# Kernel optimization log

Hardware: AMD Instinct MI355X
Metric: run time of the kernel (lower is better)

The kernel has to match this reference:

```python
import jax, jax.numpy as jnp
import numpy as np

MAX_TOTAL = 20        # max_total_size
MAX_PER_CLASS = 20    # max_output_size_per_class
SCORE_TH = 0.5        # score_threshold
IOU_TH = 0.5          # tf combined NMS default iou_threshold
K_CAND = 200          # top candidates per class considered for NMS
VARIANCES = jnp.array([0.1, 0.1, 0.2, 0.2], jnp.float32)


def setup_inputs() -> dict:
    key = jax.random.key(0)
    k1, k2, k3, k4, k5, k6 = jax.random.split(key, 6)
    B, N, C = 64, 8732, 21
    pred_deltas = jax.random.normal(k1, (B, N, 4), jnp.float32)
    pred_labels = jax.random.uniform(k2, (B, N, C), dtype=jnp.float32)
    # synthetic normalized anchors (y1,x1,y2,x2) with valid extents
    cy = jax.random.uniform(k3, (N,), dtype=jnp.float32)
    cx = jax.random.uniform(k4, (N,), dtype=jnp.float32)
    h = jax.random.uniform(k5, (N,), dtype=jnp.float32, minval=0.05, maxval=0.3)
    w = jax.random.uniform(k6, (N,), dtype=jnp.float32, minval=0.05, maxval=0.3)
    anchors = jnp.stack([cy - h / 2, cx - w / 2, cy + h / 2, cx + w / 2], axis=-1)
    return {"pred_deltas": pred_deltas, "pred_labels": pred_labels, "anchors": anchors}


def _decode(anchors, deltas):
    # anchors [N,4] (y1,x1,y2,x2); deltas [B,N,4] (dy,dx,dh,dw) -> boxes [B,N,4]
    ah = anchors[:, 2] - anchors[:, 0]
    aw = anchors[:, 3] - anchors[:, 1]
    acy = anchors[:, 0] + 0.5 * ah
    acx = anchors[:, 1] + 0.5 * aw
    cy = deltas[..., 0] * ah + acy
    cx = deltas[..., 1] * aw + acx
    h = jnp.exp(deltas[..., 2]) * ah
    w = jnp.exp(deltas[..., 3]) * aw
    return jnp.stack([cy - 0.5 * h, cx - 0.5 * w, cy + 0.5 * h, cx + 0.5 * w], axis=-1)


def _pairwise_iou(boxes):
    # boxes [K,4] -> iou [K,K]
    y1, x1, y2, x2 = boxes[:, 0], boxes[:, 1], boxes[:, 2], boxes[:, 3]
    area = (y2 - y1) * (x2 - x1)
    ih = jnp.clip(jnp.minimum(y2[:, None], y2[None, :]) - jnp.maximum(y1[:, None], y1[None, :]), 0.0)
    iw = jnp.clip(jnp.minimum(x2[:, None], x2[None, :]) - jnp.maximum(x1[:, None], x1[None, :]), 0.0)
    inter = ih * iw
    return inter / (area[:, None] + area[None, :] - inter + 1e-8)


def _nms_one_class(scores, boxes):
    # scores [N], boxes [N,4] -> (top scores [MAX_PER_CLASS], boxes [MAX_PER_CLASS,4])
    vals, idx = jax.lax.top_k(scores, K_CAND)          # sorted desc
    cboxes = boxes[idx]                                # [K,4]
    iou = _pairwise_iou(cboxes)                        # [K,K]
    valid = vals > SCORE_TH
    ar = jnp.arange(K_CAND)

    def body(i, keep):
        suppressed = jnp.any(keep & (iou[i] > IOU_TH) & (ar < i))
        return keep.at[i].set(valid[i] & ~suppressed)

    keep = jax.lax.fori_loop(0, K_CAND, body, jnp.zeros(K_CAND, dtype=bool))
    kept_scores = jnp.where(keep, vals, 0.0)
    top_vals, top_i = jax.lax.top_k(kept_scores, MAX_PER_CLASS)
    return top_vals, cboxes[top_i]


def reference(pred_deltas, pred_labels, anchors):
    deltas = pred_deltas * VARIANCES                       # variance scaling
    boxes = _decode(anchors, deltas)                       # [B,N,4]
    # zero out all class scores where argmax class == 0 (background)
    lab_map = jnp.argmax(pred_labels, axis=-1, keepdims=True)
    scores = jnp.where(lab_map != 0, pred_labels, 0.0)     # [B,N,C]

    per_class = jax.vmap(_nms_one_class, in_axes=(1, None))   # over classes
    per_batch = jax.vmap(per_class, in_axes=(0, 0))           # over batch
    cls_scores, cls_boxes = per_batch(scores, boxes)          # [B,C,P], [B,C,P,4]

    B, C, P = cls_scores.shape
    flat_scores = cls_scores.reshape(B, C * P)
    flat_boxes = cls_boxes.reshape(B, C * P, 4)
    class_ids = jnp.broadcast_to(jnp.arange(C, dtype=jnp.float32)[:, None], (C, P)).reshape(-1)

    top_vals, top_i = jax.lax.top_k(flat_scores, MAX_TOTAL)   # [B,MAX_TOTAL]
    final_boxes = jnp.take_along_axis(flat_boxes, top_i[..., None], axis=1)
    final_boxes = jnp.clip(final_boxes, 0.0, 1.0)             # combined NMS clip_boxes=True
    valid = top_vals > 0.0
    final_boxes = jnp.where(valid[..., None], final_boxes, 0.0)
    final_labels = jnp.where(valid, class_ids[top_i], 0.0)
    return final_boxes, top_vals, final_labels
```

## Files before the change

### kernel.cpp

```cpp
#include <hip/hip_runtime.h>
#include <stdint.h>

typedef unsigned long long u64;
typedef unsigned int u32;
typedef unsigned short u16;

#define BATCH 64
#define NANCH 8732
#define NCHUNK 1092
#define NCLS 21
#define KCAND 200
#define CAP 2048
#define PPC 20
#define PTOT 20
#define PRETHR 0.9f

__global__ __launch_bounds__(256) void kzero(u32* __restrict__ cnt)
{
    int i = blockIdx.x * 256 + threadIdx.x;
    if (i < BATCH * NCLS) cnt[i] = 0;
}

__global__ __launch_bounds__(256) void kdecode(
    const float* __restrict__ labels,
    unsigned char* __restrict__ msk, u64* __restrict__ lists,
    u32* __restrict__ cnt, int useT)
{
#pragma clang fp contract(off)
    const int n = blockIdx.x * 256 + threadIdx.x;
    const int b = blockIdx.y;
    const int lane = threadIdx.x & 63;
    const bool active = (n < NANCH);

    float v[NCLS];
#pragma unroll
    for (int c = 0; c < NCLS; ++c) v[c] = 0.0f;
    bool mk = false;
    if (active) {
        const float* lab = labels + ((size_t)b * NANCH + n) * NCLS;
#pragma unroll
        for (int c = 0; c < NCLS; ++c) v[c] = lab[c];
        float mx = v[0]; int am = 0;
#pragma unroll
        for (int c = 1; c < NCLS; ++c) if (v[c] > mx) { mx = v[c]; am = c; }
        mk = (am != 0);
        msk[(size_t)b * NANCH + n] = mk ? 1 : 0;
    }
    if (!useT) return;

    u32 myHits = 0;
#pragma unroll
    for (int c = 0; c < NCLS; ++c)
        if (active && mk && v[c] >= PRETHR) myHits |= (1u << c);

    u32 myCnt = 0;
#pragma unroll
    for (int c = 0; c < NCLS; ++c) {
        u64 m = __ballot((myHits >> c) & 1u);
        if (lane == c) myCnt = (u32)__popcll(m);
    }
    u32 myBase = 0;
    if (lane < NCLS) myBase = atomicAdd(&cnt[b * NCLS + lane], myCnt);

#pragma unroll
    for (int c = 0; c < NCLS; ++c) {
        u64 m = __ballot((myHits >> c) & 1u);
        u32 base = (u32)__shfl((int)myBase, c, 64);
        if ((m >> lane) & 1ull) {
            u32 rank = (u32)__popcll(m & ((1ull << lane) - 1ull));
            u32 slot = base + rank;
            if (slot < CAP)
                lists[((size_t)b * NCLS + c) * CAP + slot] =
                    ((u64)__float_as_uint(v[c]) << 32) | (u32)(~(u32)n);
        }
    }
}

__device__ __forceinline__ u64 shflxor64(u64 x, int m) {
    return (u64)__shfl_xor((long long)x, m, 64);
}

__device__ __forceinline__ void suffixFind(const u32* hist, u32* waveTot, int nb, int need,
                                           int* sSel, int* sAbove, int* sH, int* sTot,
                                           int tid, int lane, int wv)
{
    int K = (nb + 255) >> 8;
    int base = tid * K;
    u32 own = 0;
    for (int q = 0; q < K; ++q) { int bi = base + q; own += (bi < nb) ? hist[bi] : 0u; }
    u32 s = own;
#pragma unroll
    for (int d = 1; d < 64; d <<= 1) {
        u32 o = __shfl_down(s, d, 64);
        if (lane + d < 64) s += o;
    }
    if (lane == 0) waveTot[wv] = s;
    __syncthreads();
    if (tid == 0 && sTot) *sTot = (int)(waveTot[0] + waveTot[1] + waveTot[2] + waveTot[3]);
    u32 add = 0;
    for (int w = wv + 1; w < 4; ++w) add += waveTot[w];
    u32 cum = (s - own) + add;
    for (int q = K - 1; q >= 0; --q) {
        int bi = base + q;
        u32 hh = (bi < nb) ? hist[bi] : 0u;
        if (cum < (u32)need && cum + hh >= (u32)need) { *sSel = bi; *sAbove = (int)cum; *sH = (int)hh; }
        cum += hh;
    }
    __syncthreads();
}

__global__ __launch_bounds__(256) void knms(
    const float* __restrict__ labels, const unsigned char* __restrict__ msk,
    const u64* __restrict__ lists, const u32* __restrict__ cnt,
    const float* __restrict__ deltas, const float* __restrict__ anchors,
    float* __restrict__ clsScores, float* __restrict__ clsBoxes, int useT)
{
#pragma clang fp contract(off)
    __shared__ __align__(16) char smem[8192];
    u32*   hist = (u32*)smem;
    float* cbY1 = (float*)smem;
    float* cbX1 = (float*)(smem + 1024);
    float* cbY2 = (float*)(smem + 2048);
    float* cbX2 = (float*)(smem + 3072);
    float* cbAr = (float*)(smem + 4096);
    float* cVal = (float*)(smem + 5120);
    u64*   iouT = (u64*)(smem + 6144);
    __shared__ u64 candKey[256];
    __shared__ u32 waveTot[4];
    __shared__ float outS[PPC];
    __shared__ float outB[PPC * 4];
    __shared__ int sSel, sAbove, sH, sTot, sN, sKP;

    const int tid = threadIdx.x;
    const int lane = tid & 63;
    const int wv = tid >> 6;
    const int bc = blockIdx.x;
    const int b = bc / NCLS;
    const int c = bc % NCLS;

    const int nTHR = useT ? (int)cnt[bc] : -1;
    const bool fast = useT && (nTHR >= KCAND) && (nTHR <= CAP);

    if (fast) {
        const u64* lst = lists + (size_t)bc * CAP;
        u64 kr[8];
#pragma unroll
        for (int q = 0; q < 8; ++q) {
            int i = q * 256 + tid;
            kr[q] = (i < nTHR) ? lst[i] : 0ull;
        }
        for (int q = tid; q < 1024; q += 256) hist[1024 + q] = 0;
        if (tid == 0) { sSel = -1; sAbove = 0; sH = 0; sN = 0; sKP = 0; }
        __syncthreads();
#pragma unroll
        for (int q = 0; q < 8; ++q) {
            if (q * 256 + tid < nTHR) {
                float v = __uint_as_float((u32)(kr[q] >> 32));
                u32 t = (u32)(v * 65536.0f);
                atomicAdd(&hist[t >> 5], 1u);
            }
        }
        __syncthreads();
        suffixFind(hist + 1024, waveTot, 1024, KCAND, &sSel, &sAbove, &sH, nullptr, tid, lane, wv);
        int A = sAbove;
        u32 T16 = (u32)(1024 + sSel) << 5;
        int cnt2 = A + sH;

        if (cnt2 > 256) {
            if (tid < 32) hist[tid] = 0;
            if (tid == 0) { sSel = -1; sAbove = 0; sH = 0; }
            __syncthreads();
#pragma unroll
            for (int q = 0; q < 8; ++q) {
                if (q * 256 + tid < nTHR) {
                    float v = __uint_as_float((u32)(kr[q] >> 32));
                    u32 t = (u32)(v * 65536.0f);
                    if (t >= T16 && t < T16 + 32) atomicAdd(&hist[t - T16], 1u);
                }
            }
            __syncthreads();
            suffixFind(hist, waveTot, 32, KCAND - A, &sSel, &sAbove, &sH, nullptr, tid, lane, wv);
            A += sAbove;
            T16 += (u32)sSel;
        }
#pragma unroll
        for (int q = 0; q < 8; ++q) {
            if (q * 256 + tid < nTHR) {
                float v = __uint_as_float((u32)(kr[q] >> 32));
                u32 t = (u32)(v * 65536.0f);
                if (t >= T16) {
                    int slot = atomicAdd(&sN, 1);
                    if (slot < 256) candKey[slot] = kr[q];
                }
            }
        }
    } else {
        uint4 rc[5];
        for (int q = 0; q < 5; ++q) {
            int chunk = q * 256 + tid;
            u32 w4[4] = {0, 0, 0, 0};
            if (chunk < NCHUNK) {
                for (int w = 0; w < 4; ++w)
                    for (int h = 0; h < 2; ++h) {
                        int n = chunk * 8 + w * 2 + h;
                        u32 t = 0;
                        if (n < NANCH && msk[(size_t)b * NANCH + n]) {
                            float v = labels[((size_t)b * NANCH + n) * NCLS + c];
                            t = (u32)(v * 65536.0f);
                        }
                        w4[w] |= t << (16 * h);
                    }
            }
            rc[q] = make_uint4(w4[0], w4[1], w4[2], w4[3]);
        }
        for (int q = tid; q < 1024; q += 256) hist[1024 + q] = 0;
        if (tid == 0) { sSel = -1; sAbove = 0; sH = 0; sTot = 0; sN = 0; sKP = 0; }
        __syncthreads();
#pragma unroll
        for (int q = 0; q < 5; ++q) {
            if (q * 256 + tid < NCHUNK) {
                u32 w4[4] = {rc[q].x, rc[q].y, rc[q].z, rc[q].w};
#pragma unroll
                for (int w = 0; w < 4; ++w) {
                    u32 lo = w4[w] & 0xFFFFu, hi = w4[w] >> 16;
                    if (lo & 0x8000u) atomicAdd(&hist[lo >> 5], 1u);
                    if (hi & 0x8000u) atomicAdd(&hist[hi >> 5], 1u);
                }
            }
        }
        __syncthreads();
        suffixFind(hist + 1024, waveTot, 1024, KCAND, &sSel, &sAbove, &sH, &sTot, tid, lane, wv);
        int A; int cnt2; u32 T16;
        if (sTot < KCAND) { T16 = 32768u; A = 0; cnt2 = sTot; }
        else { A = sAbove; T16 = (u32)(1024 + sSel) << 5; cnt2 = A + sH; }
        if (cnt2 > 256) {
            if (tid < 32) hist[tid] = 0;
            if (tid == 0) { sSel = -1; sAbove = 0; sH = 0; }
            __syncthreads();
#pragma unroll
            for (int q = 0; q < 5; ++q) {
                if (q * 256 + tid < NCHUNK) {
                    u32 w4[4] = {rc[q].x, rc[q].y, rc[q].z, rc[q].w};
#pragma unroll
                    for (int w = 0; w < 4; ++w) {
                        u32 lo = w4[w] & 0xFFFFu, hi = w4[w] >> 16;
                        if (lo >= T16 && lo < T16 + 32) atomicAdd(&hist[lo - T16], 1u);
                        if (hi >= T16 && hi < T16 + 32) atomicAdd(&hist[hi - T16], 1u);
                    }
                }
            }
            __syncthreads();
            suffixFind(hist, waveTot, 32, KCAND - A, &sSel, &sAbove, &sH, nullptr, tid, lane, wv);
            A += sAbove;
            T16 += (u32)sSel;
        }
#pragma unroll
        for (int q = 0; q < 5; ++q) {
            int chunk = q * 256 + tid;
            if (chunk < NCHUNK) {
                u32 w4[4] = {rc[q].x, rc[q].y, rc[q].z, rc[q].w};
#pragma unroll
                for (int w = 0; w < 4; ++w) {
#pragma unroll
                    for (int h = 0; h < 2; ++h) {
                        u32 t = (h == 0) ? (w4[w] & 0xFFFFu) : (w4[w] >> 16);
                        if (t >= T16) {
                            int n = chunk * 8 + w * 2 + h;
                            float v = labels[((size_t)b * NANCH + n) * NCLS + c];
                            int slot = atomicAdd(&sN, 1);
                            if (slot < 256)
                                candKey[slot] = ((u64)__float_as_uint(v) << 32) | (u32)(~(u32)n);
                        }
                    }
                }
            }
        }
    }
    __syncthreads();
    int nc = sN; if (nc > 256) nc = 256;

    u64 x = (tid < nc) ? candKey[tid] : 0ull;
    for (int k = 2; k <= 256; k <<= 1) {
        for (int j = k >> 1; j > 0; j >>= 1) {
            u64 y;
            if (j < 64) {
                y = shflxor64(x, j);
            } else {
                __syncthreads();
                candKey[tid] = x;
                __syncthreads();
                y = candKey[tid ^ j];
            }
            bool keepMax = ((tid & k) == 0) == ((tid & j) == 0);
            u64 mx = (x > y) ? x : y;
            u64 mn = (x > y) ? y : x;
            x = keepMax ? mx : mn;
        }
    }

    float myV = __uint_as_float((u32)(x >> 32));
    float myY1 = 0.f, myX1 = 0.f, myY2 = 0.f, myX2 = 0.f, myAr = 0.f;
    u32 idx = ~(u32)x;
    if (tid < KCAND && idx < (u32)NANCH) {
        float4 d = ((const float4*)deltas)[(size_t)b * NANCH + idx];
        float4 a = ((const float4*)anchors)[idx];
        float ah = a.z - a.x, aw = a.w - a.y;
        float acy = a.x + 0.5f * ah, acx = a.y + 0.5f * aw;
        float cy = (d.x * 0.1f) * ah + acy;
        float cx = (d.y * 0.1f) * aw + acx;
        float hh2 = expf(d.z * 0.2f) * ah;
        float ww2 = expf(d.w * 0.2f) * aw;
        myY1 = cy - 0.5f * hh2; myX1 = cx - 0.5f * ww2;
        myY2 = cy + 0.5f * hh2; myX2 = cx + 0.5f * ww2;
        myAr = (myY2 - myY1) * (myX2 - myX1);
    } else {
        myV = 0.f;
    }
    __syncthreads();
    cbY1[tid] = myY1; cbX1[tid] = myX1; cbY2[tid] = myY2; cbX2[tid] = myX2;
    cbAr[tid] = myAr; cVal[tid] = myV;

    u64 k0 = 0, k1 = 0, k2 = 0, k3 = 0;
    int KPw = 0;
    for (int t0 = 0; t0 < 4; ++t0) {
        __syncthreads();
        if (sKP >= PPC) break;
        int rowBase = t0 * 64;
        int rows = KCAND - rowBase; if (rows > 64) rows = 64;
        for (int r = wv; r < rows; r += 4) {
            int i = rowBase + r;
            float y1i = cbY1[i], x1i = cbX1[i], y2i = cbY2[i], x2i = cbX2[i], ari = cbAr[i];
            for (int cg = 0; cg <= t0; ++cg) {
                int j = cg * 64 + lane;
                float ih = fminf(y2i, cbY2[j]) - fmaxf(y1i, cbY1[j]);
                ih = fmaxf(ih, 0.0f);
                float iw = fminf(x2i, cbX2[j]) - fmaxf(x1i, cbX1[j]);
                iw = fmaxf(iw, 0.0f);
                float inter = ih * iw;
                float iou = inter / (ari + cbAr[j] - inter + 1e-8f);
                u64 bal = __ballot(iou > 0.5f);
                if (lane == 0) iouT[r * 4 + cg] = bal;
            }
        }
        __syncthreads();
        if (tid < 64) {
            int i = rowBase + lane;
            u64 r0 = 0, r1 = 0, r2 = 0, r3 = 0;
            bool vld = false;
            if (lane < rows) {
                r0 = iouT[lane * 4 + 0]; r1 = iouT[lane * 4 + 1];
                r2 = iouT[lane * 4 + 2]; r3 = iouT[lane * 4 + 3];
                vld = cVal[i] > 0.5f;
            }
            for (int l = 0; l < rows; ++l) {
                int mydec = (vld && !((k0 & r0) | (k1 & r1) | (k2 & r2) | (k3 & r3))) ? 1 : 0;
                int d = __shfl(mydec, l, 64);
                if (d) {
                    u64 bit = 1ull << l;
                    if (t0 == 0) k0 |= bit; else if (t0 == 1) k1 |= bit;
                    else if (t0 == 2) k2 |= bit; else k3 |= bit;
                    ++KPw;
                    if (KPw >= PPC) break;
                }
            }
            if (tid == 0) sKP = KPw;
        }
    }
    __syncthreads();

    if (tid < PPC) outS[tid] = 0.0f;
    if (tid < PPC * 4) outB[tid] = 0.0f;
    __syncthreads();

    if (tid < 64) {
        int base = 0;
#pragma unroll
        for (int chunk = 0; chunk < 4; ++chunk) {
            u64 kw = (chunk == 0) ? k0 : (chunk == 1) ? k1 : (chunk == 2) ? k2 : k3;
            int i = chunk * 64 + tid;
            bool kept = ((kw >> tid) & 1ull) != 0;
            int rank = base + (int)__popcll(kw & ((1ull << tid) - 1ull));
            if (kept && rank < PPC && i < KCAND) {
                outS[rank] = cVal[i];
                outB[rank * 4 + 0] = cbY1[i];
                outB[rank * 4 + 1] = cbX1[i];
                outB[rank * 4 + 2] = cbY2[i];
                outB[rank * 4 + 3] = cbX2[i];
            }
            base += (int)__popcll(kw);
        }
    }
    __syncthreads();
    if (tid < PPC) clsScores[(size_t)bc * PPC + tid] = outS[tid];
    if (tid < PPC * 4) clsBoxes[(size_t)bc * PPC * 4 + tid] = outB[tid];
}

__global__ __launch_bounds__(512) void kmerge(
    const float* __restrict__ clsScores, const float* __restrict__ clsBoxes,
    float* __restrict__ out)
{
#pragma clang fp contract(off)
    __shared__ u64 key[512];
    const int tid = threadIdx.x;
    const int b = blockIdx.x;
    const int F = NCLS * PPC;
    u64 kk = 0;
    if (tid < F) {
        float v = clsScores[(size_t)b * F + tid];
        kk = ((u64)__float_as_uint(v) << 32) | (u32)(~(u32)tid);
    }
    key[tid] = kk;
    for (int k = 2; k <= 512; k <<= 1)
        for (int j = k >> 1; j > 0; j >>= 1) {
            __syncthreads();
            int ixj = tid ^ j;
            if (ixj > tid) {
                u64 a = key[tid], bb = key[ixj];
                if (((tid & k) == 0) ? (a < bb) : (a > bb)) { key[tid] = bb; key[ixj] = a; }
            }
        }
    __syncthreads();
    if (tid < PTOT) {
        u64 kx = key[tid];
        float v = __uint_as_float((u32)(kx >> 32));
        u32 f = ~((u32)kx);
        bool valid = (v > 0.0f) && (f < (u32)F);
        float cls = valid ? (float)(f / PPC) : 0.0f;
        float* oB = out;
        float* oV = out + (size_t)BATCH * PTOT * 4;
        float* oL = oV + (size_t)BATCH * PTOT;
#pragma unroll
        for (int q = 0; q < 4; ++q) {
            float xq = 0.0f;
            if (valid) {
                xq = clsBoxes[((size_t)b * F + f) * 4 + q];
                xq = fminf(fmaxf(xq, 0.0f), 1.0f);
            }
            oB[((size_t)b * PTOT + tid) * 4 + q] = xq;
        }
        oV[(size_t)b * PTOT + tid] = v;
        oL[(size_t)b * PTOT + tid] = cls;
    }
}

extern "C" void kernel_launch(void* const* d_in, const int* in_sizes, int n_in,
                              void* d_out, int out_size, void* d_ws, size_t ws_size,
                              hipStream_t stream)
{
    const float* deltas  = (const float*)d_in[0];
    const float* labels  = (const float*)d_in[1];
    const float* anchors = (const float*)d_in[2];
    float* out = (float*)d_out;
    char* ws = (char*)d_ws;

    const size_t mskOff  = 0;
    const size_t cntOff  = 558848;
    const size_t csOff   = 564480;
    const size_t cbOff   = 672000;
    const size_t listOff = 1102336;
    const size_t needT   = 23122432;

    unsigned char* msk = (unsigned char*)(ws + mskOff);
    u32* cnt         = (u32*)(ws + cntOff);
    float* clsScores = (float*)(ws + csOff);
    float* clsBoxes  = (float*)(ws + cbOff);
    u64* lists       = (u64*)(ws + listOff);
    int useT = (ws_size >= needT) ? 1 : 0;

    if (useT) kzero<<<(BATCH * NCLS + 255) / 256, 256, 0, stream>>>(cnt);
    dim3 gA((NANCH + 255) / 256, BATCH);
    kdecode<<<gA, 256, 0, stream>>>(labels, msk, lists, cnt, useT);
    knms<<<BATCH * NCLS, 256, 0, stream>>>(labels, msk, lists, cnt, deltas, anchors,
                                           clsScores, clsBoxes, useT);
    kmerge<<<BATCH, 512, 0, stream>>>(clsScores, clsBoxes, out);
}
```

Measured before the change: 58.55 us.

## Run per-class NMS on a single wavefront to drop block barriers

Each (batch, class) NMS problem now runs on one 64-lane wavefront, with two problems packed per block, so every block-wide barrier becomes a wave-local LDS wait. The histogram suffix search, the candidate bitonic sort (four keys per lane via shuffles) and the greedy suppression loop (broadcasting each kept box by shuffle and testing IoU against register-held boxes) are all rewritten for this layout. The merge kernel's bitonic sort also switches to shuffles for strides below 64. The goal is to cut sync and LDS traffic, at the cost of fewer threads per problem and longer serial loops within each wave.

```diff
diff --git a/kernel.cpp b/kernel.cpp
--- a/kernel.cpp
+++ b/kernel.cpp
@@ -7,13 +7,17 @@
 
 #define BATCH 64
 #define NANCH 8732
-#define NCHUNK 1092
+#define NPAD16 8736
 #define NCLS 21
 #define KCAND 200
 #define CAP 2048
 #define PPC 20
 #define PTOT 20
 #define PRETHR 0.9f
+#define WPB 2
+
+#define WFENCE() do { asm volatile("s_waitcnt lgkmcnt(0)" ::: "memory"); \
+                      __builtin_amdgcn_sched_barrier(0); } while (0)
 
 __global__ __launch_bounds__(256) void kzero(u32* __restrict__ cnt)
 {
@@ -80,350 +84,280 @@
     return (u64)__shfl_xor((long long)x, m, 64);
 }
 
-__device__ __forceinline__ void suffixFind(const u32* hist, u32* waveTot, int nb, int need,
-                                           int* sSel, int* sAbove, int* sH, int* sTot,
-                                           int tid, int lane, int wv)
-{
-    int K = (nb + 255) >> 8;
-    int base = tid * K;
-    u32 own = 0;
-    for (int q = 0; q < K; ++q) { int bi = base + q; own += (bi < nb) ? hist[bi] : 0u; }
+__device__ __forceinline__ void waveSuffixFind(const u32* hist, int need, int lane,
+                                               int& sel, int& above, int& h, int& tot)
+{
+    u32 bins[16]; u32 own = 0;
+#pragma unroll
+    for (int q = 0; q < 16; ++q) { bins[q] = hist[lane * 16 + q]; own += bins[q]; }
     u32 s = own;
 #pragma unroll
     for (int d = 1; d < 64; d <<= 1) {
-        u32 o = __shfl_down(s, d, 64);
+        u32 o = (u32)__shfl_down((int)s, d, 64);
         if (lane + d < 64) s += o;
     }
-    if (lane == 0) waveTot[wv] = s;
-    __syncthreads();
-    if (tid == 0 && sTot) *sTot = (int)(waveTot[0] + waveTot[1] + waveTot[2] + waveTot[3]);
-    u32 add = 0;
-    for (int w = wv + 1; w < 4; ++w) add += waveTot[w];
-    u32 cum = (s - own) + add;
-    for (int q = K - 1; q >= 0; --q) {
-        int bi = base + q;
-        u32 hh = (bi < nb) ? hist[bi] : 0u;
-        if (cum < (u32)need && cum + hh >= (u32)need) { *sSel = bi; *sAbove = (int)cum; *sH = (int)hh; }
+    tot = __shfl((int)s, 0, 64);
+    u32 cum = s - own;
+    int lsel = -1, labove = 0, lh = 0;
+#pragma unroll
+    for (int q = 15; q >= 0; --q) {
+        u32 hh = bins[q];
+        if (cum < (u32)need && cum + hh >= (u32)need) { lsel = lane * 16 + q; labove = (int)cum; lh = (int)hh; }
         cum += hh;
     }
-    __syncthreads();
-}
-
-__global__ __launch_bounds__(256) void knms(
+    u64 pk = (lsel >= 0) ? (((u64)(u32)(lsel + 1) << 48) | ((u64)(u32)labove << 24) | (u32)lh) : 0ull;
+#pragma unroll
+    for (int d = 1; d < 64; d <<= 1) { u64 o = shflxor64(pk, d); if (o > pk) pk = o; }
+    sel = (int)(pk >> 48) - 1;
+    above = (int)((pk >> 24) & 0xFFFFFFull);
+    h = (int)(pk & 0xFFFFFFull);
+}
+
+#define CMPXP(a, b, km) { u64 mx_ = (a) > (b) ? (a) : (b); u64 mn_ = (a) > (b) ? (b) : (a); \
+                          (a) = (km) ? mx_ : mn_; (b) = (km) ? mn_ : mx_; }
+
+#define WKEYS   0
+#define WHIST   17536
+#define WCAND   21632
+#define WOUTS   23680
+#define WOUTB   23760
+#define WSCNT   24080
+#define WSTRIDE 24128
+
+__global__ __launch_bounds__(64 * WPB) void knms(
     const float* __restrict__ labels, const unsigned char* __restrict__ msk,
     const u64* __restrict__ lists, const u32* __restrict__ cnt,
     const float* __restrict__ deltas, const float* __restrict__ anchors,
     float* __restrict__ clsScores, float* __restrict__ clsBoxes, int useT)
 {
 #pragma clang fp contract(off)
-    __shared__ __align__(16) char smem[8192];
-    u32*   hist = (u32*)smem;
-    float* cbY1 = (float*)smem;
-    float* cbX1 = (float*)(smem + 1024);
-    float* cbY2 = (float*)(smem + 2048);
-    float* cbX2 = (float*)(smem + 3072);
-    float* cbAr = (float*)(smem + 4096);
-    float* cVal = (float*)(smem + 5120);
-    u64*   iouT = (u64*)(smem + 6144);
-    __shared__ u64 candKey[256];
-    __shared__ u32 waveTot[4];
-    __shared__ float outS[PPC];
-    __shared__ float outB[PPC * 4];
-    __shared__ int sSel, sAbove, sH, sTot, sN, sKP;
-
-    const int tid = threadIdx.x;
-    const int lane = tid & 63;
-    const int wv = tid >> 6;
-    const int bc = blockIdx.x;
+    __shared__ __align__(16) char smem[WPB * WSTRIDE];
+    const int lane = threadIdx.x & 63;
+    const int wv = threadIdx.x >> 6;
+    const int bc = blockIdx.x * WPB + wv;
     const int b = bc / NCLS;
     const int c = bc % NCLS;
+    char* wm = smem + wv * WSTRIDE;
+    u64* keys = (u64*)(wm + WKEYS);
+    u16* t16s = (u16*)(wm + WKEYS);
+    u32* hist = (u32*)(wm + WHIST);
+    u64* cand = (u64*)(wm + WCAND);
+    float* outS = (float*)(wm + WOUTS);
+    float* outB = (float*)(wm + WOUTB);
+    u32* scnt = (u32*)(wm + WSCNT);
 
     const int nTHR = useT ? (int)cnt[bc] : -1;
     const bool fast = useT && (nTHR >= KCAND) && (nTHR <= CAP);
 
+#pragma unroll
+    for (int q = 0; q < 16; ++q) hist[lane + q * 64] = 0;
+#pragma unroll
+    for (int q = 0; q < 4; ++q) cand[lane + q * 64] = 0;
+    if (lane < PPC) outS[lane] = 0.0f;
+#pragma unroll
+    for (int q = 0; q < 2; ++q) { int l = lane + q * 64; if (l < PPC * 4) outB[l] = 0.0f; }
+    if (lane == 0) *scnt = 0;
+    WFENCE();
+
+    int A = 0, cnt2 = 0, tot = 0;
+    u32 T16 = 0;
     if (fast) {
         const u64* lst = lists + (size_t)bc * CAP;
-        u64 kr[8];
-#pragma unroll
-        for (int q = 0; q < 8; ++q) {
-            int i = q * 256 + tid;
-            kr[q] = (i < nTHR) ? lst[i] : 0ull;
-        }
-        for (int q = tid; q < 1024; q += 256) hist[1024 + q] = 0;
-        if (tid == 0) { sSel = -1; sAbove = 0; sH = 0; sN = 0; sKP = 0; }
-        __syncthreads();
-#pragma unroll
-        for (int q = 0; q < 8; ++q) {
-            if (q * 256 + tid < nTHR) {
-                float v = __uint_as_float((u32)(kr[q] >> 32));
-                u32 t = (u32)(v * 65536.0f);
-                atomicAdd(&hist[t >> 5], 1u);
-            }
-        }
-        __syncthreads();
-        suffixFind(hist + 1024, waveTot, 1024, KCAND, &sSel, &sAbove, &sH, nullptr, tid, lane, wv);
-        int A = sAbove;
-        u32 T16 = (u32)(1024 + sSel) << 5;
-        int cnt2 = A + sH;
-
+        for (int i = lane; i < nTHR; i += 64) {
+            u64 kk = lst[i];
+            keys[i] = kk;
+            u32 t = (u32)(__uint_as_float((u32)(kk >> 32)) * 65536.0f);
+            atomicAdd(&hist[(t >> 5) - 1024], 1u);
+        }
+        WFENCE();
+        int sel, above, h;
+        waveSuffixFind(hist, KCAND, lane, sel, above, h, tot);
+        A = above; T16 = (u32)(1024 + sel) << 5; cnt2 = A + h;
         if (cnt2 > 256) {
-            if (tid < 32) hist[tid] = 0;
-            if (tid == 0) { sSel = -1; sAbove = 0; sH = 0; }
-            __syncthreads();
-#pragma unroll
-            for (int q = 0; q < 8; ++q) {
-                if (q * 256 + tid < nTHR) {
-                    float v = __uint_as_float((u32)(kr[q] >> 32));
-                    u32 t = (u32)(v * 65536.0f);
-                    if (t >= T16 && t < T16 + 32) atomicAdd(&hist[t - T16], 1u);
-                }
-            }
-            __syncthreads();
-            suffixFind(hist, waveTot, 32, KCAND - A, &sSel, &sAbove, &sH, nullptr, tid, lane, wv);
-            A += sAbove;
-            T16 += (u32)sSel;
-        }
-#pragma unroll
-        for (int q = 0; q < 8; ++q) {
-            if (q * 256 + tid < nTHR) {
-                float v = __uint_as_float((u32)(kr[q] >> 32));
-                u32 t = (u32)(v * 65536.0f);
-                if (t >= T16) {
-                    int slot = atomicAdd(&sN, 1);
-                    if (slot < 256) candKey[slot] = kr[q];
-                }
-            }
+#pragma unroll
+            for (int q = 0; q < 16; ++q) hist[lane + q * 64] = 0;
+            WFENCE();
+            for (int i = lane; i < nTHR; i += 64) {
+                u32 t = (u32)(__uint_as_float((u32)(keys[i] >> 32)) * 65536.0f);
+                if (t >= T16 && t < T16 + 32) atomicAdd(&hist[t - T16], 1u);
+            }
+            WFENCE();
+            int s2, a2, h2, t2;
+            waveSuffixFind(hist, KCAND - A, lane, s2, a2, h2, t2);
+            A += a2; T16 += (u32)s2; cnt2 = A + h2;
+        }
+        for (int i = lane; i < nTHR; i += 64) {
+            u64 kk = keys[i];
+            u32 t = (u32)(__uint_as_float((u32)(kk >> 32)) * 65536.0f);
+            if (t >= T16) { u32 slot = atomicAdd(scnt, 1u); if (slot < 256) cand[slot] = kk; }
         }
     } else {
-        uint4 rc[5];
-        for (int q = 0; q < 5; ++q) {
-            int chunk = q * 256 + tid;
-            u32 w4[4] = {0, 0, 0, 0};
-            if (chunk < NCHUNK) {
-                for (int w = 0; w < 4; ++w)
-                    for (int h = 0; h < 2; ++h) {
-                        int n = chunk * 8 + w * 2 + h;
-                        u32 t = 0;
-                        if (n < NANCH && msk[(size_t)b * NANCH + n]) {
-                            float v = labels[((size_t)b * NANCH + n) * NCLS + c];
-                            t = (u32)(v * 65536.0f);
-                        }
-                        w4[w] |= t << (16 * h);
-                    }
-            }
-            rc[q] = make_uint4(w4[0], w4[1], w4[2], w4[3]);
-        }
-        for (int q = tid; q < 1024; q += 256) hist[1024 + q] = 0;
-        if (tid == 0) { sSel = -1; sAbove = 0; sH = 0; sTot = 0; sN = 0; sKP = 0; }
-        __syncthreads();
-#pragma unroll
-        for (int q = 0; q < 5; ++q) {
-            if (q * 256 + tid < NCHUNK) {
-                u32 w4[4] = {rc[q].x, rc[q].y, rc[q].z, rc[q].w};
-#pragma unroll
-                for (int w = 0; w < 4; ++w) {
-                    u32 lo = w4[w] & 0xFFFFu, hi = w4[w] >> 16;
-                    if (lo & 0x8000u) atomicAdd(&hist[lo >> 5], 1u);
-                    if (hi & 0x8000u) atomicAdd(&hist[hi >> 5], 1u);
-                }
-            }
-        }
-        __syncthreads();
-        suffixFind(hist + 1024, waveTot, 1024, KCAND, &sSel, &sAbove, &sH, &sTot, tid, lane, wv);
-        int A; int cnt2; u32 T16;
-        if (sTot < KCAND) { T16 = 32768u; A = 0; cnt2 = sTot; }
-        else { A = sAbove; T16 = (u32)(1024 + sSel) << 5; cnt2 = A + sH; }
+        for (int i = lane; i < NPAD16; i += 64) {
+            u32 t = 0;
+            if (i < NANCH && msk[(size_t)b * NANCH + i]) {
+                float v = labels[((size_t)b * NANCH + i) * NCLS + c];
+                t = (u32)(v * 65536.0f);
+            }
+            t16s[i] = (u16)t;
+            if (t >= 32768u) atomicAdd(&hist[(t >> 5) - 1024], 1u);
+        }
+        WFENCE();
+        int sel, above, h;
+        waveSuffixFind(hist, KCAND, lane, sel, above, h, tot);
+        if (tot < KCAND) { T16 = 32768u; A = 0; cnt2 = tot; }
+        else { A = above; T16 = (u32)(1024 + sel) << 5; cnt2 = A + h; }
         if (cnt2 > 256) {
-            if (tid < 32) hist[tid] = 0;
-            if (tid == 0) { sSel = -1; sAbove = 0; sH = 0; }
-            __syncthreads();
-#pragma unroll
-            for (int q = 0; q < 5; ++q) {
-                if (q * 256 + tid < NCHUNK) {
-                    u32 w4[4] = {rc[q].x, rc[q].y, rc[q].z, rc[q].w};
-#pragma unroll
-                    for (int w = 0; w < 4; ++w) {
-                        u32 lo = w4[w] & 0xFFFFu, hi = w4[w] >> 16;
-                        if (lo >= T16 && lo < T16 + 32) atomicAdd(&hist[lo - T16], 1u);
-                        if (hi >= T16 && hi < T16 + 32) atomicAdd(&hist[hi - T16], 1u);
-                    }
-                }
-            }
-            __syncthreads();
-            suffixFind(hist, waveTot, 32, KCAND - A, &sSel, &sAbove, &sH, nullptr, tid, lane, wv);
-            A += sAbove;
-            T16 += (u32)sSel;
-        }
-#pragma unroll
-        for (int q = 0; q < 5; ++q) {
-            int chunk = q * 256 + tid;
-            if (chunk < NCHUNK) {
-                u32 w4[4] = {rc[q].x, rc[q].y, rc[q].z, rc[q].w};
-#pragma unroll
-                for (int w = 0; w < 4; ++w) {
-#pragma unroll
-                    for (int h = 0; h < 2; ++h) {
-                        u32 t = (h == 0) ? (w4[w] & 0xFFFFu) : (w4[w] >> 16);
-                        if (t >= T16) {
-                            int n = chunk * 8 + w * 2 + h;
-                            float v = labels[((size_t)b * NANCH + n) * NCLS + c];
-                            int slot = atomicAdd(&sN, 1);
-                            if (slot < 256)
-                                candKey[slot] = ((u64)__float_as_uint(v) << 32) | (u32)(~(u32)n);
-                        }
-                    }
-                }
-            }
-        }
-    }
-    __syncthreads();
-    int nc = sN; if (nc > 256) nc = 256;
-
-    u64 x = (tid < nc) ? candKey[tid] : 0ull;
+#pragma unroll
+            for (int q = 0; q < 16; ++q) hist[lane + q * 64] = 0;
+            WFENCE();
+            for (int i = lane; i < NPAD16; i += 64) {
+                u32 t = t16s[i];
+                if (t >= T16 && t < T16 + 32) atomicAdd(&hist[t - T16], 1u);
+            }
+            WFENCE();
+            int s2, a2, h2, t2;
+            waveSuffixFind(hist, KCAND - A, lane, s2, a2, h2, t2);
+            A += a2; T16 += (u32)s2; cnt2 = A + h2;
+        }
+        for (int i = lane; i < NPAD16; i += 64) {
+            u32 t = t16s[i];
+            if (t >= T16) {
+                float v = labels[((size_t)b * NANCH + i) * NCLS + c];
+                u32 slot = atomicAdd(scnt, 1u);
+                if (slot < 256) cand[slot] = ((u64)__float_as_uint(v) << 32) | (u32)(~(u32)i);
+            }
+        }
+    }
+    WFENCE();
+
+    u64 x[4];
+#pragma unroll
+    for (int s = 0; s < 4; ++s) x[s] = cand[s * 64 + lane];
     for (int k = 2; k <= 256; k <<= 1) {
-        for (int j = k >> 1; j > 0; j >>= 1) {
+        if (k == 128) { CMPXP(x[0], x[1], true); CMPXP(x[2], x[3], false); }
+        if (k == 256) { CMPXP(x[0], x[2], true); CMPXP(x[1], x[3], true);
+                        CMPXP(x[0], x[1], true); CMPXP(x[2], x[3], true); }
+        int j0 = (k >> 1) > 32 ? 32 : (k >> 1);
+        for (int j = j0; j >= 1; j >>= 1) {
+#pragma unroll
+            for (int s = 0; s < 4; ++s) {
+                u64 y = shflxor64(x[s], j);
+                int idx = (s << 6) | lane;
+                bool keepMax = ((idx & k) == 0) == ((lane & j) == 0);
+                u64 mx = x[s] > y ? x[s] : y;
+                u64 mn = x[s] > y ? y : x[s];
+                x[s] = keepMax ? mx : mn;
+            }
+        }
+    }
+
+    float y1r[4], x1r[4], y2r[4], x2r[4], arr_[4], vvr[4];
+    u32 vbits = 0;
+#pragma unroll
+    for (int s = 0; s < 4; ++s) {
+        float v = __uint_as_float((u32)(x[s] >> 32));
+        u32 idx = ~(u32)x[s];
+        y1r[s] = 0.f; x1r[s] = 0.f; y2r[s] = 0.f; x2r[s] = 0.f; arr_[s] = 0.f; vvr[s] = 0.f;
+        int gi = (s << 6) | lane;
+        if (gi < KCAND && idx < (u32)NANCH) {
+            float4 d = ((const float4*)deltas)[(size_t)b * NANCH + idx];
+            float4 a = ((const float4*)anchors)[idx];
+            float ah = a.z - a.x, aw = a.w - a.y;
+            float acy = a.x + 0.5f * ah, acx = a.y + 0.5f * aw;
+            float cy = (d.x * 0.1f) * ah + acy;
+            float cx = (d.y * 0.1f) * aw + acx;
+            float hh2 = expf(d.z * 0.2f) * ah;
+            float ww2 = expf(d.w * 0.2f) * aw;
+            y1r[s] = cy - 0.5f * hh2; x1r[s] = cx - 0.5f * ww2;
+            y2r[s] = cy + 0.5f * hh2; x2r[s] = cx + 0.5f * ww2;
+            arr_[s] = (y2r[s] - y1r[s]) * (x2r[s] - x1r[s]);
+            vvr[s] = v;
+            if (v > 0.5f) vbits |= (1u << s);
+        }
+    }
+
+#define BCAST(s) do { \
+        bY1 = __shfl(y1r[s], ln, 64); bX1 = __shfl(x1r[s], ln, 64); \
+        bY2 = __shfl(y2r[s], ln, 64); bX2 = __shfl(x2r[s], ln, 64); \
+        bAr = __shfl(arr_[s], ln, 64); \
+        if (lane == ln) { \
+            outS[kept] = vvr[s]; \
+            outB[kept * 4 + 0] = y1r[s]; outB[kept * 4 + 1] = x1r[s]; \
+            outB[kept * 4 + 2] = y2r[s]; outB[kept * 4 + 3] = x2r[s]; \
+        } } while (0)
+
+    u32 sup = 0;
+    int kept = 0;
+    for (int i = 0; i < KCAND && kept < PPC; ++i) {
+        int sl = i >> 6, ln = i & 63;
+        u32 vb = (u32)__shfl((int)vbits, ln, 64);
+        u32 sw = (u32)__shfl((int)sup, ln, 64);
+        if (((vb >> sl) & 1u) && !((sw >> sl) & 1u)) {
+            float bY1, bX1, bY2, bX2, bAr;
+            switch (sl) {
+                case 0: BCAST(0); break;
+                case 1: BCAST(1); break;
+                case 2: BCAST(2); break;
+                default: BCAST(3); break;
+            }
+#pragma unroll
+            for (int s2 = 0; s2 < 4; ++s2) {
+                float ih = fminf(bY2, y2r[s2]) - fmaxf(bY1, y1r[s2]);
+                ih = fmaxf(ih, 0.0f);
+                float iw = fminf(bX2, x2r[s2]) - fmaxf(bX1, x1r[s2]);
+                iw = fmaxf(iw, 0.0f);
+                float inter = ih * iw;
+                float iou = inter / (bAr + arr_[s2] - inter + 1e-8f);
+                if (iou > 0.5f) sup |= (1u << s2);
+            }
+            ++kept;
+        }
+    }
+#undef BCAST
+    WFENCE();
+
+    if (lane < PPC) clsScores[(size_t)bc * PPC + lane] = outS[lane];
+#pragma unroll
+    for (int q = 0; q < 2; ++q) {
+        int l = lane + q * 64;
+        if (l < PPC * 4) clsBoxes[(size_t)bc * PPC * 4 + l] = outB[l];
+    }
+}
+
+__global__ __launch_bounds__(512) void kmerge(
+    const float* __restrict__ clsScores, const float* __restrict__ clsBoxes,
+    float* __restrict__ out)
+{
+#pragma clang fp contract(off)
+    __shared__ u64 key[512];
+    const int tid = threadIdx.x;
+    const int b = blockIdx.x;
+    const int F = NCLS * PPC;
+    u64 x = 0;
+    if (tid < F) {
+        float v = clsScores[(size_t)b * F + tid];
+        x = ((u64)__float_as_uint(v) << 32) | (u32)(~(u32)tid);
+    }
+    for (int k = 2; k <= 512; k <<= 1) {
+        for (int j = k >> 1; j >= 1; j >>= 1) {
             u64 y;
             if (j < 64) {
                 y = shflxor64(x, j);
             } else {
                 __syncthreads();
-                candKey[tid] = x;
+                key[tid] = x;
                 __syncthreads();
-                y = candKey[tid ^ j];
+                y = key[tid ^ j];
             }
             bool keepMax = ((tid & k) == 0) == ((tid & j) == 0);
-            u64 mx = (x > y) ? x : y;
-            u64 mn = (x > y) ? y : x;
+            u64 mx = x > y ? x : y;
+            u64 mn = x > y ? y : x;
             x = keepMax ? mx : mn;
         }
     }
-
-    float myV = __uint_as_float((u32)(x >> 32));
-    float myY1 = 0.f, myX1 = 0.f, myY2 = 0.f, myX2 = 0.f, myAr = 0.f;
-    u32 idx = ~(u32)x;
-    if (tid < KCAND && idx < (u32)NANCH) {
-        float4 d = ((const float4*)deltas)[(size_t)b * NANCH + idx];
-        float4 a = ((const float4*)anchors)[idx];
-        float ah = a.z - a.x, aw = a.w - a.y;
-        float acy = a.x + 0.5f * ah, acx = a.y + 0.5f * aw;
-        float cy = (d.x * 0.1f) * ah + acy;
-        float cx = (d.y * 0.1f) * aw + acx;
-        float hh2 = expf(d.z * 0.2f) * ah;
-        float ww2 = expf(d.w * 0.2f) * aw;
-        myY1 = cy - 0.5f * hh2; myX1 = cx - 0.5f * ww2;
-        myY2 = cy + 0.5f * hh2; myX2 = cx + 0.5f * ww2;
-        myAr = (myY2 - myY1) * (myX2 - myX1);
-    } else {
-        myV = 0.f;
-    }
-    __syncthreads();
-    cbY1[tid] = myY1; cbX1[tid] = myX1; cbY2[tid] = myY2; cbX2[tid] = myX2;
-    cbAr[tid] = myAr; cVal[tid] = myV;
-
-    u64 k0 = 0, k1 = 0, k2 = 0, k3 = 0;
-    int KPw = 0;
-    for (int t0 = 0; t0 < 4; ++t0) {
-        __syncthreads();
-        if (sKP >= PPC) break;
-        int rowBase = t0 * 64;
-        int rows = KCAND - rowBase; if (rows > 64) rows = 64;
-        for (int r = wv; r < rows; r += 4) {
-            int i = rowBase + r;
-            float y1i = cbY1[i], x1i = cbX1[i], y2i = cbY2[i], x2i = cbX2[i], ari = cbAr[i];
-            for (int cg = 0; cg <= t0; ++cg) {
-                int j = cg * 64 + lane;
-                float ih = fminf(y2i, cbY2[j]) - fmaxf(y1i, cbY1[j]);
-                ih = fmaxf(ih, 0.0f);
-                float iw = fminf(x2i, cbX2[j]) - fmaxf(x1i, cbX1[j]);
-                iw = fmaxf(iw, 0.0f);
-                float inter = ih * iw;
-                float iou = inter / (ari + cbAr[j] - inter + 1e-8f);
-                u64 bal = __ballot(iou > 0.5f);
-                if (lane == 0) iouT[r * 4 + cg] = bal;
-            }
-        }
-        __syncthreads();
-        if (tid < 64) {
-            int i = rowBase + lane;
-            u64 r0 = 0, r1 = 0, r2 = 0, r3 = 0;
-            bool vld = false;
-            if (lane < rows) {
-                r0 = iouT[lane * 4 + 0]; r1 = iouT[lane * 4 + 1];
-                r2 = iouT[lane * 4 + 2]; r3 = iouT[lane * 4 + 3];
-                vld = cVal[i] > 0.5f;
-            }
-            for (int l = 0; l < rows; ++l) {
-                int mydec = (vld && !((k0 & r0) | (k1 & r1) | (k2 & r2) | (k3 & r3))) ? 1 : 0;
-                int d = __shfl(mydec, l, 64);
-                if (d) {
-                    u64 bit = 1ull << l;
-                    if (t0 == 0) k0 |= bit; else if (t0 == 1) k1 |= bit;
-                    else if (t0 == 2) k2 |= bit; else k3 |= bit;
-                    ++KPw;
-                    if (KPw >= PPC) break;
-                }
-            }
-            if (tid == 0) sKP = KPw;
-        }
-    }
-    __syncthreads();
-
-    if (tid < PPC) outS[tid] = 0.0f;
-    if (tid < PPC * 4) outB[tid] = 0.0f;
-    __syncthreads();
-
-    if (tid < 64) {
-        int base = 0;
-#pragma unroll
-        for (int chunk = 0; chunk < 4; ++chunk) {
-            u64 kw = (chunk == 0) ? k0 : (chunk == 1) ? k1 : (chunk == 2) ? k2 : k3;
-            int i = chunk * 64 + tid;
-            bool kept = ((kw >> tid) & 1ull) != 0;
-            int rank = base + (int)__popcll(kw & ((1ull << tid) - 1ull));
-            if (kept && rank < PPC && i < KCAND) {
-                outS[rank] = cVal[i];
-                outB[rank * 4 + 0] = cbY1[i];
-                outB[rank * 4 + 1] = cbX1[i];
-                outB[rank * 4 + 2] = cbY2[i];
-                outB[rank * 4 + 3] = cbX2[i];
-            }
-            base += (int)__popcll(kw);
-        }
-    }
-    __syncthreads();
-    if (tid < PPC) clsScores[(size_t)bc * PPC + tid] = outS[tid];
-    if (tid < PPC * 4) clsBoxes[(size_t)bc * PPC * 4 + tid] = outB[tid];
-}
-
-__global__ __launch_bounds__(512) void kmerge(
-    const float* __restrict__ clsScores, const float* __restrict__ clsBoxes,
-    float* __restrict__ out)
-{
-#pragma clang fp contract(off)
-    __shared__ u64 key[512];
-    const int tid = threadIdx.x;
-    const int b = blockIdx.x;
-    const int F = NCLS * PPC;
-    u64 kk = 0;
-    if (tid < F) {
-        float v = clsScores[(size_t)b * F + tid];
-        kk = ((u64)__float_as_uint(v) << 32) | (u32)(~(u32)tid);
-    }
-    key[tid] = kk;
-    for (int k = 2; k <= 512; k <<= 1)
-        for (int j = k >> 1; j > 0; j >>= 1) {
-            __syncthreads();
-            int ixj = tid ^ j;
-            if (ixj > tid) {
-                u64 a = key[tid], bb = key[ixj];
-                if (((tid & k) == 0) ? (a < bb) : (a > bb)) { key[tid] = bb; key[ixj] = a; }
-            }
-        }
-    __syncthreads();
     if (tid < PTOT) {
-        u64 kx = key[tid];
-        float v = __uint_as_float((u32)(kx >> 32));
-        u32 f = ~((u32)kx);
+        float v = __uint_as_float((u32)(x >> 32));
+        u32 f = ~((u32)x);
         bool valid = (v > 0.0f) && (f < (u32)F);
         float cls = valid ? (float)(f / PPC) : 0.0f;
         float* oB = out;
@@ -470,7 +404,7 @@
     if (useT) kzero<<<(BATCH * NCLS + 255) / 256, 256, 0, stream>>>(cnt);
     dim3 gA((NANCH + 255) / 256, BATCH);
     kdecode<<<gA, 256, 0, stream>>>(labels, msk, lists, cnt, useT);
-    knms<<<BATCH * NCLS, 256, 0, stream>>>(labels, msk, lists, cnt, deltas, anchors,
-                                           clsScores, clsBoxes, useT);
+    knms<<<(BATCH * NCLS) / WPB, 64 * WPB, 0, stream>>>(labels, msk, lists, cnt, deltas, anchors,
+                                                        clsScores, clsBoxes, useT);
     kmerge<<<BATCH, 512, 0, stream>>>(clsScores, clsBoxes, out);
 }
```

Result: slower. 69.32 us (+18.4%).

## Fuse per-batch merge into NMS kernel via last-block arrival counter

Applied to the files above, without the earlier changes.

Adds a per-batch arrival counter so the last class block finishing NMS for a batch performs the top-20 merge. It does this with a 512-element bitonic sort held in registers, shared memory and shuffles, which removes the separate kmerge launch when the workspace path is used. It also loads the 21 label floats per anchor as five 16-byte vector copies plus one scalar. The fused path relies on threadfence and atomic-load ordering, and it adds sort work to the tail of one block per batch. The vector loads assume alignment that the 84-byte row stride does not always give.

```diff
diff --git a/kernel.cpp b/kernel.cpp
--- a/kernel.cpp
+++ b/kernel.cpp
@@ -15,10 +15,11 @@
 #define PTOT 20
 #define PRETHR 0.9f
 
-__global__ __launch_bounds__(256) void kzero(u32* __restrict__ cnt)
+__global__ __launch_bounds__(256) void kzero(u32* __restrict__ cnt, u32* __restrict__ arrive)
 {
     int i = blockIdx.x * 256 + threadIdx.x;
     if (i < BATCH * NCLS) cnt[i] = 0;
+    if (i < BATCH) arrive[i] = 0;
 }
 
 __global__ __launch_bounds__(256) void kdecode(
@@ -38,8 +39,15 @@
     bool mk = false;
     if (active) {
         const float* lab = labels + ((size_t)b * NANCH + n) * NCLS;
-#pragma unroll
-        for (int c = 0; c < NCLS; ++c) v[c] = lab[c];
+        float4 t[5];
+#pragma unroll
+        for (int q = 0; q < 5; ++q) __builtin_memcpy(&t[q], lab + q * 4, 16);
+#pragma unroll
+        for (int q = 0; q < 5; ++q) {
+            v[q * 4 + 0] = t[q].x; v[q * 4 + 1] = t[q].y;
+            v[q * 4 + 2] = t[q].z; v[q * 4 + 3] = t[q].w;
+        }
+        v[20] = lab[20];
         float mx = v[0]; int am = 0;
 #pragma unroll
         for (int c = 1; c < NCLS; ++c) if (v[c] > mx) { mx = v[c]; am = c; }
@@ -113,7 +121,8 @@
     const float* __restrict__ labels, const unsigned char* __restrict__ msk,
     const u64* __restrict__ lists, const u32* __restrict__ cnt,
     const float* __restrict__ deltas, const float* __restrict__ anchors,
-    float* __restrict__ clsScores, float* __restrict__ clsBoxes, int useT)
+    float* __restrict__ clsScores, float* __restrict__ clsBoxes,
+    u32* __restrict__ arrive, float* __restrict__ out, int useT)
 {
 #pragma clang fp contract(off)
     __shared__ __align__(16) char smem[8192];
@@ -129,7 +138,7 @@
     __shared__ u32 waveTot[4];
     __shared__ float outS[PPC];
     __shared__ float outB[PPC * 4];
-    __shared__ int sSel, sAbove, sH, sTot, sN, sKP;
+    __shared__ int sSel, sAbove, sH, sTot, sN, sKP, sOld;
 
     const int tid = threadIdx.x;
     const int lane = tid & 63;
@@ -393,6 +402,91 @@
     __syncthreads();
     if (tid < PPC) clsScores[(size_t)bc * PPC + tid] = outS[tid];
     if (tid < PPC * 4) clsBoxes[(size_t)bc * PPC * 4 + tid] = outB[tid];
+
+    if (!useT) return;
+
+    __syncthreads();
+    if (tid == 0) {
+        __threadfence();
+        sOld = (int)atomicAdd(&arrive[b], 1u);
+    }
+    __syncthreads();
+    if (sOld != NCLS - 1) return;
+    __threadfence();
+
+    const int F = NCLS * PPC;
+    u64* skey = (u64*)smem;
+    u64 x0, x1;
+    {
+        float v0 = __hip_atomic_load(&clsScores[(size_t)b * F + tid],
+                                     __ATOMIC_RELAXED, __HIP_MEMORY_SCOPE_AGENT);
+        x0 = ((u64)__float_as_uint(v0) << 32) | (u32)(~(u32)tid);
+        int i1 = tid + 256;
+        if (i1 < F) {
+            float v1 = __hip_atomic_load(&clsScores[(size_t)b * F + i1],
+                                         __ATOMIC_RELAXED, __HIP_MEMORY_SCOPE_AGENT);
+            x1 = ((u64)__float_as_uint(v1) << 32) | (u32)(~(u32)i1);
+        } else x1 = 0ull;
+    }
+    for (int k = 2; k <= 512; k <<= 1) {
+        for (int j = k >> 1; j >= 1; j >>= 1) {
+            if (j >= 256) {
+                bool km = ((tid & k) == 0) == (((tid) & j & 255) == 0);
+                u64 mx = x0 > x1 ? x0 : x1, mn = x0 > x1 ? x1 : x0;
+                x0 = km ? mx : mn; x1 = km ? mn : mx;
+            } else if (j >= 64) {
+                __syncthreads();
+                skey[tid] = x0; skey[tid + 256] = x1;
+                __syncthreads();
+                u64 y0 = skey[tid ^ j], y1 = skey[(tid ^ j) + 256];
+                {
+                    bool km = ((tid & k) == 0) == ((tid & j) == 0);
+                    u64 mx = x0 > y0 ? x0 : y0, mn = x0 > y0 ? y0 : x0;
+                    x0 = km ? mx : mn;
+                }
+                {
+                    int v1i = tid + 256;
+                    bool km = ((v1i & k) == 0) == ((tid & j) == 0);
+                    u64 mx = x1 > y1 ? x1 : y1, mn = x1 > y1 ? y1 : x1;
+                    x1 = km ? mx : mn;
+                }
+            } else {
+                u64 y0 = shflxor64(x0, j), y1 = shflxor64(x1, j);
+                {
+                    bool km = ((tid & k) == 0) == ((tid & j) == 0);
+                    u64 mx = x0 > y0 ? x0 : y0, mn = x0 > y0 ? y0 : x0;
+                    x0 = km ? mx : mn;
+                }
+                {
+                    int v1i = tid + 256;
+                    bool km = ((v1i & k) == 0) == ((tid & j) == 0);
+                    u64 mx = x1 > y1 ? x1 : y1, mn = x1 > y1 ? y1 : x1;
+                    x1 = km ? mx : mn;
+                }
+            }
+        }
+    }
+    if (tid < PTOT) {
+        float v = __uint_as_float((u32)(x0 >> 32));
+        u32 f = ~((u32)x0);
+        bool valid = (v > 0.0f) && (f < (u32)F);
+        float cls = valid ? (float)(f / PPC) : 0.0f;
+        float* oB = out;
+        float* oV = out + (size_t)BATCH * PTOT * 4;
+        float* oL = oV + (size_t)BATCH * PTOT;
+#pragma unroll
+        for (int q = 0; q < 4; ++q) {
+            float xq = 0.0f;
+            if (valid) {
+                xq = __hip_atomic_load(&clsBoxes[((size_t)b * F + f) * 4 + q],
+                                       __ATOMIC_RELAXED, __HIP_MEMORY_SCOPE_AGENT);
+                xq = fminf(fmaxf(xq, 0.0f), 1.0f);
+            }
+            oB[((size_t)b * PTOT + tid) * 4 + q] = xq;
+        }
+        oV[(size_t)b * PTOT + tid] = v;
+        oL[(size_t)b * PTOT + tid] = cls;
+    }
 }
 
 __global__ __launch_bounds__(512) void kmerge(
@@ -455,6 +549,7 @@
 
     const size_t mskOff  = 0;
     const size_t cntOff  = 558848;
+    const size_t arrOff  = 564224;
     const size_t csOff   = 564480;
     const size_t cbOff   = 672000;
     const size_t listOff = 1102336;
@@ -462,15 +557,16 @@
 
     unsigned char* msk = (unsigned char*)(ws + mskOff);
     u32* cnt         = (u32*)(ws + cntOff);
+    u32* arrive      = (u32*)(ws + arrOff);
     float* clsScores = (float*)(ws + csOff);
     float* clsBoxes  = (float*)(ws + cbOff);
     u64* lists       = (u64*)(ws + listOff);
     int useT = (ws_size >= needT) ? 1 : 0;
 
-    if (useT) kzero<<<(BATCH * NCLS + 255) / 256, 256, 0, stream>>>(cnt);
+    if (useT) kzero<<<(BATCH * NCLS + 255) / 256, 256, 0, stream>>>(cnt, arrive);
     dim3 gA((NANCH + 255) / 256, BATCH);
     kdecode<<<gA, 256, 0, stream>>>(labels, msk, lists, cnt, useT);
     knms<<<BATCH * NCLS, 256, 0, stream>>>(labels, msk, lists, cnt, deltas, anchors,
-                                           clsScores, clsBoxes, useT);
-    kmerge<<<BATCH, 512, 0, stream>>>(clsScores, clsBoxes, out);
-}
+                                           clsScores, clsBoxes, arrive, out, useT);
+    if (!useT) kmerge<<<BATCH, 512, 0, stream>>>(clsScores, clsBoxes, out);
+}
```

Result: slower. 97.63 us (+66.7%).

## Replace histogram top-k select with full 1024-element register bitonic sort

Applied to the files above, without the earlier changes.

On the fast path (per-class candidate list of at most 1024 entries), the two-level histogram radix-select, atomic compaction and separate 256-wide sort are replaced by one bitonic sort of up to 1024 keys held four per thread. The top 200 then come straight out of thread registers. The aim is to avoid shared-memory atomic contention and the suffix-scan barriers, at the cost of more compare-exchange stages. Lists between 1025 and 2048 entries now drop to the slow rescan path. The zeroing kernel is also replaced by hipMemsetAsync.

```diff
diff --git a/kernel.cpp b/kernel.cpp
--- a/kernel.cpp
+++ b/kernel.cpp
@@ -11,15 +11,10 @@
 #define NCLS 21
 #define KCAND 200
 #define CAP 2048
+#define SORTN 1024
 #define PPC 20
 #define PTOT 20
 #define PRETHR 0.9f
-
-__global__ __launch_bounds__(256) void kzero(u32* __restrict__ cnt)
-{
-    int i = blockIdx.x * 256 + threadIdx.x;
-    if (i < BATCH * NCLS) cnt[i] = 0;
-}
 
 __global__ __launch_bounds__(256) void kdecode(
     const float* __restrict__ labels,
@@ -80,6 +75,9 @@
     return (u64)__shfl_xor((long long)x, m, 64);
 }
 
+#define CMPXP(a, b, km) { u64 mx_ = (a) > (b) ? (a) : (b); u64 mn_ = (a) > (b) ? (b) : (a); \
+                          (a) = (km) ? mx_ : mn_; (b) = (km) ? mn_ : mx_; }
+
 __device__ __forceinline__ void suffixFind(const u32* hist, u32* waveTot, int nb, int need,
                                            int* sSel, int* sAbove, int* sH, int* sTot,
                                            int tid, int lane, int wv)
@@ -117,6 +115,7 @@
 {
 #pragma clang fp contract(off)
     __shared__ __align__(16) char smem[8192];
+    u64*   sbuf = (u64*)smem;
     u32*   hist = (u32*)smem;
     float* cbY1 = (float*)smem;
     float* cbX1 = (float*)(smem + 1024);
@@ -139,61 +138,51 @@
     const int c = bc % NCLS;
 
     const int nTHR = useT ? (int)cnt[bc] : -1;
-    const bool fast = useT && (nTHR >= KCAND) && (nTHR <= CAP);
-
+    const bool fast = useT && (nTHR >= KCAND) && (nTHR <= SORTN);
+
+    u64 x;
     if (fast) {
+        if (tid == 0) sKP = 0;
         const u64* lst = lists + (size_t)bc * CAP;
-        u64 kr[8];
-#pragma unroll
-        for (int q = 0; q < 8; ++q) {
-            int i = q * 256 + tid;
-            kr[q] = (i < nTHR) ? lst[i] : 0ull;
-        }
-        for (int q = tid; q < 1024; q += 256) hist[1024 + q] = 0;
-        if (tid == 0) { sSel = -1; sAbove = 0; sH = 0; sN = 0; sKP = 0; }
-        __syncthreads();
-#pragma unroll
-        for (int q = 0; q < 8; ++q) {
-            if (q * 256 + tid < nTHR) {
-                float v = __uint_as_float((u32)(kr[q] >> 32));
-                u32 t = (u32)(v * 65536.0f);
-                atomicAdd(&hist[t >> 5], 1u);
-            }
-        }
-        __syncthreads();
-        suffixFind(hist + 1024, waveTot, 1024, KCAND, &sSel, &sAbove, &sH, nullptr, tid, lane, wv);
-        int A = sAbove;
-        u32 T16 = (u32)(1024 + sSel) << 5;
-        int cnt2 = A + sH;
-
-        if (cnt2 > 256) {
-            if (tid < 32) hist[tid] = 0;
-            if (tid == 0) { sSel = -1; sAbove = 0; sH = 0; }
-            __syncthreads();
-#pragma unroll
-            for (int q = 0; q < 8; ++q) {
-                if (q * 256 + tid < nTHR) {
-                    float v = __uint_as_float((u32)(kr[q] >> 32));
-                    u32 t = (u32)(v * 65536.0f);
-                    if (t >= T16 && t < T16 + 32) atomicAdd(&hist[t - T16], 1u);
-                }
-            }
-            __syncthreads();
-            suffixFind(hist, waveTot, 32, KCAND - A, &sSel, &sAbove, &sH, nullptr, tid, lane, wv);
-            A += sAbove;
-            T16 += (u32)sSel;
-        }
-#pragma unroll
-        for (int q = 0; q < 8; ++q) {
-            if (q * 256 + tid < nTHR) {
-                float v = __uint_as_float((u32)(kr[q] >> 32));
-                u32 t = (u32)(v * 65536.0f);
-                if (t >= T16) {
-                    int slot = atomicAdd(&sN, 1);
-                    if (slot < 256) candKey[slot] = kr[q];
-                }
-            }
-        }
+        u64 xr[4];
+#pragma unroll
+        for (int s = 0; s < 4; ++s) {
+            int i = s * 256 + tid;
+            xr[s] = (i < nTHR) ? lst[i] : 0ull;
+        }
+        for (int k = 2; k <= SORTN; k <<= 1) {
+            for (int j = k >> 1; j >= 1; j >>= 1) {
+                if (j == 512) {
+                    CMPXP(xr[0], xr[2], true); CMPXP(xr[1], xr[3], true);
+                } else if (j == 256) {
+                    bool km23 = (k == 1024);
+                    CMPXP(xr[0], xr[1], true); CMPXP(xr[2], xr[3], km23);
+                } else if (j >= 64) {
+                    __syncthreads();
+#pragma unroll
+                    for (int s = 0; s < 4; ++s) sbuf[s * 256 + tid] = xr[s];
+                    __syncthreads();
+#pragma unroll
+                    for (int s = 0; s < 4; ++s) {
+                        u64 y = sbuf[s * 256 + (tid ^ j)];
+                        bool km = (((s * 256 + tid) & k) == 0) == ((tid & j) == 0);
+                        u64 mx = xr[s] > y ? xr[s] : y;
+                        u64 mn = xr[s] > y ? y : xr[s];
+                        xr[s] = km ? mx : mn;
+                    }
+                } else {
+#pragma unroll
+                    for (int s = 0; s < 4; ++s) {
+                        u64 y = shflxor64(xr[s], j);
+                        bool km = (((s * 256 + tid) & k) == 0) == ((tid & j) == 0);
+                        u64 mx = xr[s] > y ? xr[s] : y;
+                        u64 mn = xr[s] > y ? y : xr[s];
+                        xr[s] = km ? mx : mn;
+                    }
+                }
+            }
+        }
+        x = xr[0];
     } else {
         uint4 rc[5];
         for (int q = 0; q < 5; ++q) {
@@ -275,26 +264,25 @@
                 }
             }
         }
-    }
-    __syncthreads();
-    int nc = sN; if (nc > 256) nc = 256;
-
-    u64 x = (tid < nc) ? candKey[tid] : 0ull;
-    for (int k = 2; k <= 256; k <<= 1) {
-        for (int j = k >> 1; j > 0; j >>= 1) {
-            u64 y;
-            if (j < 64) {
-                y = shflxor64(x, j);
-            } else {
-                __syncthreads();
-                candKey[tid] = x;
-                __syncthreads();
-                y = candKey[tid ^ j];
-            }
-            bool keepMax = ((tid & k) == 0) == ((tid & j) == 0);
-            u64 mx = (x > y) ? x : y;
-            u64 mn = (x > y) ? y : x;
-            x = keepMax ? mx : mn;
+        __syncthreads();
+        int nc = sN; if (nc > 256) nc = 256;
+        x = (tid < nc) ? candKey[tid] : 0ull;
+        for (int k = 2; k <= 256; k <<= 1) {
+            for (int j = k >> 1; j > 0; j >>= 1) {
+                u64 y;
+                if (j < 64) {
+                    y = shflxor64(x, j);
+                } else {
+                    __syncthreads();
+                    candKey[tid] = x;
+                    __syncthreads();
+                    y = candKey[tid ^ j];
+                }
+                bool keepMax = ((tid & k) == 0) == ((tid & j) == 0);
+                u64 mx = (x > y) ? x : y;
+                u64 mn = (x > y) ? y : x;
+                x = keepMax ? mx : mn;
+            }
         }
     }
 
@@ -467,7 +455,7 @@
     u64* lists       = (u64*)(ws + listOff);
     int useT = (ws_size >= needT) ? 1 : 0;
 
-    if (useT) kzero<<<(BATCH * NCLS + 255) / 256, 256, 0, stream>>>(cnt);
+    if (useT) hipMemsetAsync(cnt, 0, BATCH * NCLS * sizeof(u32), stream);
     dim3 gA((NANCH + 255) / 256, BATCH);
     kdecode<<<gA, 256, 0, stream>>>(labels, msk, lists, cnt, useT);
     knms<<<BATCH * NCLS, 256, 0, stream>>>(labels, msk, lists, cnt, deltas, anchors,
```

Measured after the change: 84.56 us. 1.44x slower.
